# Kernel tuning notes

Measured on AMD Instinct MI355X. Metric: run time of the kernel, lower is better.

The kernel has to match this reference:

```python
import jax, jax.numpy as jnp
import numpy as np

N_NODES = 100000
N_EDGES = 1600000
NODE_IN = 64
EDGE_DIM = 32
NODE_OUT = 64


def setup_inputs() -> dict:
    key = jax.random.key(0)
    ks = jax.random.split(key, 8)
    return {
        "nfeats": jax.random.normal(ks[0], (N_NODES, NODE_IN), dtype=jnp.float32),
        "efeats": jax.random.normal(ks[1], (N_EDGES, EDGE_DIM), dtype=jnp.float32),
        "src": jax.random.randint(ks[2], (N_EDGES,), 0, N_NODES, dtype=jnp.int32),
        "dst": jax.random.randint(ks[3], (N_EDGES,), 0, N_NODES, dtype=jnp.int32),
        "W_msg_w": jax.random.normal(ks[4], (NODE_IN + EDGE_DIM, NODE_OUT), dtype=jnp.float32) * 0.1,
        "W_msg_b": jax.random.normal(ks[5], (NODE_OUT,), dtype=jnp.float32) * 0.1,
        "W_apply_w": jax.random.normal(ks[6], (NODE_IN + NODE_OUT, NODE_OUT), dtype=jnp.float32) * 0.1,
        "W_apply_b": jax.random.normal(ks[7], (NODE_OUT,), dtype=jnp.float32) * 0.1,
    }


def reference(nfeats, efeats, src, dst, W_msg_w, W_msg_b, W_apply_w, W_apply_b):
    n_nodes = nfeats.shape[0]
    # message: gather source node features, concat edge features, linear
    m = jnp.concatenate([nfeats[src], efeats], axis=-1) @ W_msg_w + W_msg_b  # [E, node_out]
    # per-destination mean (DGL fn.mean); zero for isolated nodes
    s = jax.ops.segment_sum(m, dst, num_segments=n_nodes)                     # [N, node_out]
    cnt = jax.ops.segment_sum(jnp.ones((m.shape[0],), m.dtype), dst, num_segments=n_nodes)
    h_neigh = s / jnp.maximum(cnt, 1.0)[:, None]
    # apply: concat self features with aggregated messages, linear, activation
    h = jnp.concatenate([nfeats, h_neigh], axis=-1) @ W_apply_w + W_apply_b   # [N, node_out]
    return jax.nn.relu(h)
```

## Files before the change

### kernel.cpp

```cpp
#include <hip/hip_runtime.h>
#include <hip/hip_bf16.h>

#define NN 100000
#define NE 1600000
#define NBIN 782
#define CAP  2560
#define EPB  8192
#define NBLKE 196

#define OFF_BINSZ   100004
#define OFF_BINBASE 100788
#define OFF_MASK    101572
#define OFF_EINFO   300520
#define OFF_G       3500520
#define OFF_HM      OFF_G
#define OFF_OM      (OFF_G + 153272)
#define OFF_WCOMB   13100520
#define OFF_BMW     13110760

__global__ __launch_bounds__(256) void k_cvt(const float4* __restrict__ nf4,
                                             uint4* __restrict__ nfb) {
  int t = blockIdx.x * 256 + threadIdx.x;
  float4 a = nf4[t * 2], b = nf4[t * 2 + 1];
  uint4 o;
  o.x = ((uint)__bfloat16_as_ushort(__float2bfloat16(a.x))) |
        ((uint)__bfloat16_as_ushort(__float2bfloat16(a.y)) << 16);
  o.y = ((uint)__bfloat16_as_ushort(__float2bfloat16(a.z))) |
        ((uint)__bfloat16_as_ushort(__float2bfloat16(a.w)) << 16);
  o.z = ((uint)__bfloat16_as_ushort(__float2bfloat16(b.x))) |
        ((uint)__bfloat16_as_ushort(__float2bfloat16(b.y)) << 16);
  o.w = ((uint)__bfloat16_as_ushort(__float2bfloat16(b.z))) |
        ((uint)__bfloat16_as_ushort(__float2bfloat16(b.w)) << 16);
  nfb[t] = o;
}

__global__ __launch_bounds__(256) void k_bhist(const int4* __restrict__ dst4,
                                               int* __restrict__ hm) {
  __shared__ int h[NBIN];
  int b = blockIdx.x, t = threadIdx.x;
  for (int i = t; i < NBIN; i += 256) h[i] = 0;
  __syncthreads();
  int e0 = b * EPB;
#pragma unroll
  for (int i = 0; i < EPB / 1024; ++i) {
    int f = i * 256 + t;
    int e = e0 + f * 4;
    if (e < NE) {
      int4 d = dst4[(e0 >> 2) + f];
      atomicAdd(&h[d.x >> 7], 1);
      atomicAdd(&h[d.y >> 7], 1);
      atomicAdd(&h[d.z >> 7], 1);
      atomicAdd(&h[d.w >> 7], 1);
    }
  }
  __syncthreads();
  for (int i = t; i < NBIN; i += 256) hm[b * NBIN + i] = h[i];
}

__global__ __launch_bounds__(256) void k_bscan(const int* __restrict__ hm,
                                               int* __restrict__ om,
                                               int* __restrict__ binsz) {
  int w = (blockIdx.x * 256 + threadIdx.x) >> 6;
  int lane = threadIdx.x & 63;
  if (w >= NBIN) return;
  int carry = 0;
  for (int base = 0; base < NBLKE; base += 64) {
    int b = base + lane;
    int v = (b < NBLKE) ? hm[b * NBIN + w] : 0;
    int inc = v;
#pragma unroll
    for (int off = 1; off < 64; off <<= 1) {
      int x = __shfl_up(inc, off);
      if (lane >= off) inc += x;
    }
    if (b < NBLKE) om[b * NBIN + w] = carry + inc - v;
    carry += __shfl(inc, 63);
  }
  if (lane == 0) binsz[w] = carry;
}

__global__ __launch_bounds__(1024) void k_binscan(const int* __restrict__ binsz,
                                                  int* __restrict__ binbase) {
  __shared__ int s[1024];
  int t = threadIdx.x;
  int v = (t < NBIN) ? binsz[t] : 0;
  s[t] = v; __syncthreads();
#pragma unroll
  for (int off = 1; off < 1024; off <<= 1) {
    int x = (t >= off) ? s[t - off] : 0;
    __syncthreads();
    s[t] += x;
    __syncthreads();
  }
  if (t <= NBIN) binbase[t] = s[t] - v;
}

__global__ __launch_bounds__(256) void k_bplace(
    const int4* __restrict__ src4, const int4* __restrict__ dst4,
    const int* __restrict__ om, const int* __restrict__ binbase,
    int2* __restrict__ einfo) {
  __shared__ int2 buf[EPB];
  __shared__ int hstart[1024];
  __shared__ int hcur[1024];
  __shared__ int obase[NBIN];
  __shared__ int tscan[256];
  int b = blockIdx.x, t = threadIdx.x;
  int e0 = b * EPB;
  for (int i = t; i < 1024; i += 256) hcur[i] = 0;
  for (int i = t; i < NBIN; i += 256) obase[i] = binbase[i] + om[b * NBIN + i];
  __syncthreads();
#pragma unroll
  for (int i = 0; i < EPB / 1024; ++i) {
    int f = i * 256 + t;
    int e = e0 + f * 4;
    if (e < NE) {
      int4 d = dst4[(e0 >> 2) + f];
      atomicAdd(&hcur[d.x >> 7], 1);
      atomicAdd(&hcur[d.y >> 7], 1);
      atomicAdd(&hcur[d.z >> 7], 1);
      atomicAdd(&hcur[d.w >> 7], 1);
    }
  }
  __syncthreads();
  int base4 = t * 4;
  int v0 = hcur[base4], v1 = hcur[base4 + 1], v2 = hcur[base4 + 2], v3 = hcur[base4 + 3];
  int s = v0 + v1 + v2 + v3;
  tscan[t] = s;
  __syncthreads();
#pragma unroll
  for (int off = 1; off < 256; off <<= 1) {
    int x = (t >= off) ? tscan[t - off] : 0;
    __syncthreads();
    tscan[t] += x;
    __syncthreads();
  }
  int texcl = tscan[t] - s;
  hstart[base4]     = texcl;
  hstart[base4 + 1] = texcl + v0;
  hstart[base4 + 2] = texcl + v0 + v1;
  hstart[base4 + 3] = texcl + v0 + v1 + v2;
  __syncthreads();
  for (int i = t; i < 1024; i += 256) hcur[i] = hstart[i];
  __syncthreads();
#pragma unroll
  for (int i = 0; i < EPB / 1024; ++i) {
    int f = i * 256 + t;
    int e = e0 + f * 4;
    if (e < NE) {
      int4 d = dst4[(e0 >> 2) + f];
      int4 sv = src4[(e0 >> 2) + f];
      int p0 = atomicAdd(&hcur[d.x >> 7], 1);
      int p1 = atomicAdd(&hcur[d.y >> 7], 1);
      int p2 = atomicAdd(&hcur[d.z >> 7], 1);
      int p3 = atomicAdd(&hcur[d.w >> 7], 1);
      buf[p0] = make_int2(sv.x | ((d.x & 127) << 20), (e)     | ((d.x >> 7) << 21));
      buf[p1] = make_int2(sv.y | ((d.y & 127) << 20), (e + 1) | ((d.y >> 7) << 21));
      buf[p2] = make_int2(sv.z | ((d.z & 127) << 20), (e + 2) | ((d.z >> 7) << 21));
      buf[p3] = make_int2(sv.w | ((d.w & 127) << 20), (e + 3) | ((d.w >> 7) << 21));
    }
  }
  __syncthreads();
  int nE = NE - e0; if (nE > EPB) nE = EPB;
  for (int i = t; i < nE; i += 256) {
    int2 r = buf[i];
    int bin = (unsigned)r.y >> 21;
    int pos = obase[bin] + (i - hstart[bin]);
    einfo[pos] = make_int2(r.x, r.y & 0x1FFFFF);
  }
}

__global__ __launch_bounds__(512, 8) void k_sortgather(
    const uint* __restrict__ nfb, const float* __restrict__ ef,
    const int2* __restrict__ einfo, const int* __restrict__ binbase,
    float* __restrict__ g, float* __restrict__ mask) {
  __shared__ int2 buf[CAP];
  __shared__ int hist[128];
  __shared__ int excl[128];
  __shared__ int sstart[129];
  int b = blockIdx.x, t = threadIdx.x;
  int base = binbase[b];
  int nE = binbase[b + 1] - base;
  int nS = nE < CAP ? nE : CAP;
  if (t < 128) hist[t] = 0;
  __syncthreads();
  int2 myreg[5];
#pragma unroll
  for (int i = 0; i < 5; ++i) {
    int idx = i * 512 + t;
    if (idx < nS) {
      myreg[i] = einfo[base + idx];
      atomicAdd(&hist[(myreg[i].x >> 20) & 127], 1);
    } else {
      myreg[i] = make_int2(-1, 0);
    }
  }
  __syncthreads();
  int myc = 0;
  if (t < 128) { myc = hist[t]; excl[t] = myc; }
  __syncthreads();
#pragma unroll
  for (int off = 1; off < 128; off <<= 1) {
    int x = 0;
    if (t < 128 && t >= off) x = excl[t - off];
    __syncthreads();
    if (t < 128) excl[t] += x;
    __syncthreads();
  }
  if (t < 128) {
    int node = b * 128 + t;
    if (node < NN) mask[node] = myc ? 1.f : 0.f;
    sstart[t] = excl[t] - myc;
    hist[t] = excl[t] - myc;
    if (t == 127) sstart[128] = excl[127];
  }
  __syncthreads();
#pragma unroll
  for (int i = 0; i < 5; ++i) {
    if (myreg[i].x >= 0) {
      int dl = (myreg[i].x >> 20) & 127;
      int p = atomicAdd(&hist[dl], 1);
      buf[p] = make_int2(myreg[i].x & 0xFFFFF, myreg[i].y);
    }
  }
  __syncthreads();
  int wv = t >> 6, lane = t & 63;
  bool hi = lane >= 32;
  int l32 = lane & 31;
  for (int k = 0; k < 16; ++k) {
    int dl = wv * 16 + k;
    int node = b * 128 + dl;
    if (node >= NN) break;
    int beg = sstart[dl], end = sstart[dl + 1];
    int deg = end - beg;
    float a0x = 0.f, a0y = 0.f, a1 = 0.f;
    int j = beg;
    for (; j + 16 <= end; j += 16) {
      int2 q0 = buf[j + 0];
      int2 q1 = buf[j + 1];
      int2 q2 = buf[j + 2];
      int2 q3 = buf[j + 3];
      int2 q4 = buf[j + 4];
      int2 q5 = buf[j + 5];
      int2 q6 = buf[j + 6];
      int2 q7 = buf[j + 7];
      int2 q8 = buf[j + 8];
      int2 q9 = buf[j + 9];
      int2 qa = buf[j + 10];
      int2 qb = buf[j + 11];
      int2 qc = buf[j + 12];
      int2 qd = buf[j + 13];
      int2 qe = buf[j + 14];
      int2 qf = buf[j + 15];
      int n0 = hi ? q1.x : q0.x;
      int n1 = hi ? q3.x : q2.x;
      int n2 = hi ? q5.x : q4.x;
      int n3 = hi ? q7.x : q6.x;
      int n4 = hi ? q9.x : q8.x;
      int n5 = hi ? qb.x : qa.x;
      int n6 = hi ? qd.x : qc.x;
      int n7 = hi ? qf.x : qe.x;
      int e0 = hi ? q1.y : q0.y;
      int e1 = hi ? q3.y : q2.y;
      int e2 = hi ? q5.y : q4.y;
      int e3 = hi ? q7.y : q6.y;
      int e4 = hi ? q9.y : q8.y;
      int e5 = hi ? qb.y : qa.y;
      int e6 = hi ? qd.y : qc.y;
      int e7 = hi ? qf.y : qe.y;
      uint u0 = nfb[n0 * 32 + l32];
      uint u1 = nfb[n1 * 32 + l32];
      uint u2 = nfb[n2 * 32 + l32];
      uint u3 = nfb[n3 * 32 + l32];
      uint u4 = nfb[n4 * 32 + l32];
      uint u5 = nfb[n5 * 32 + l32];
      uint u6 = nfb[n6 * 32 + l32];
      uint u7 = nfb[n7 * 32 + l32];
      float w0 = ef[e0 * 32 + l32];
      float w1 = ef[e1 * 32 + l32];
      float w2 = ef[e2 * 32 + l32];
      float w3 = ef[e3 * 32 + l32];
      float w4 = ef[e4 * 32 + l32];
      float w5 = ef[e5 * 32 + l32];
      float w6 = ef[e6 * 32 + l32];
      float w7 = ef[e7 * 32 + l32];
      a0x += __uint_as_float(u0 << 16) + __uint_as_float(u1 << 16)
           + __uint_as_float(u2 << 16) + __uint_as_float(u3 << 16)
           + __uint_as_float(u4 << 16) + __uint_as_float(u5 << 16)
           + __uint_as_float(u6 << 16) + __uint_as_float(u7 << 16);
      a0y += __uint_as_float(u0 & 0xFFFF0000u) + __uint_as_float(u1 & 0xFFFF0000u)
           + __uint_as_float(u2 & 0xFFFF0000u) + __uint_as_float(u3 & 0xFFFF0000u)
           + __uint_as_float(u4 & 0xFFFF0000u) + __uint_as_float(u5 & 0xFFFF0000u)
           + __uint_as_float(u6 & 0xFFFF0000u) + __uint_as_float(u7 & 0xFFFF0000u);
      a1 += ((w0 + w1) + (w2 + w3)) + ((w4 + w5) + (w6 + w7));
    }
    for (; j + 8 <= end; j += 8) {
      int2 q0 = buf[j + 0];
      int2 q1 = buf[j + 1];
      int2 q2 = buf[j + 2];
      int2 q3 = buf[j + 3];
      int2 q4 = buf[j + 4];
      int2 q5 = buf[j + 5];
      int2 q6 = buf[j + 6];
      int2 q7 = buf[j + 7];
      int n0 = hi ? q1.x : q0.x;
      int n1 = hi ? q3.x : q2.x;
      int n2 = hi ? q5.x : q4.x;
      int n3 = hi ? q7.x : q6.x;
      int e0 = hi ? q1.y : q0.y;
      int e1 = hi ? q3.y : q2.y;
      int e2 = hi ? q5.y : q4.y;
      int e3 = hi ? q7.y : q6.y;
      uint u0 = nfb[n0 * 32 + l32];
      uint u1 = nfb[n1 * 32 + l32];
      uint u2 = nfb[n2 * 32 + l32];
      uint u3 = nfb[n3 * 32 + l32];
      float w0 = ef[e0 * 32 + l32];
      float w1 = ef[e1 * 32 + l32];
      float w2 = ef[e2 * 32 + l32];
      float w3 = ef[e3 * 32 + l32];
      a0x += __uint_as_float(u0 << 16) + __uint_as_float(u1 << 16)
           + __uint_as_float(u2 << 16) + __uint_as_float(u3 << 16);
      a0y += __uint_as_float(u0 & 0xFFFF0000u) + __uint_as_float(u1 & 0xFFFF0000u)
           + __uint_as_float(u2 & 0xFFFF0000u) + __uint_as_float(u3 & 0xFFFF0000u);
      a1 += (w0 + w1) + (w2 + w3);
    }
    for (; j + 4 <= end; j += 4) {
      int2 q0 = buf[j + 0];
      int2 q1 = buf[j + 1];
      int2 q2 = buf[j + 2];
      int2 q3 = buf[j + 3];
      int n0 = hi ? q1.x : q0.x;
      int n1 = hi ? q3.x : q2.x;
      int e0 = hi ? q1.y : q0.y;
      int e1 = hi ? q3.y : q2.y;
      uint u0 = nfb[n0 * 32 + l32];
      uint u1 = nfb[n1 * 32 + l32];
      float w0 = ef[e0 * 32 + l32];
      float w1 = ef[e1 * 32 + l32];
      a0x += __uint_as_float(u0 << 16) + __uint_as_float(u1 << 16);
      a0y += __uint_as_float(u0 & 0xFFFF0000u) + __uint_as_float(u1 & 0xFFFF0000u);
      a1 += w0 + w1;
    }
    for (; j + 2 <= end; j += 2) {
      int2 q0 = buf[j];
      int2 q1 = buf[j + 1];
      int n0 = hi ? q1.x : q0.x;
      int e0 = hi ? q1.y : q0.y;
      uint u0 = nfb[n0 * 32 + l32];
      float w0 = ef[e0 * 32 + l32];
      a0x += __uint_as_float(u0 << 16);
      a0y += __uint_as_float(u0 & 0xFFFF0000u);
      a1 += w0;
    }
    if (j < end) {
      int2 q0 = buf[j];
      if (!hi) {
        uint u0 = nfb[q0.x * 32 + l32];
        a0x += __uint_as_float(u0 << 16);
        a0y += __uint_as_float(u0 & 0xFFFF0000u);
        a1 += ef[q0.y * 32 + l32];
      }
    }
    a0x += __shfl_xor(a0x, 32);
    a0y += __shfl_xor(a0y, 32);
    a1 += __shfl_down(a1, 32);
    float inv = deg > 0 ? 1.f / (float)deg : 0.f;
    if (!hi) {
      *(float2*)&g[node * 96 + l32 * 2] = make_float2(a0x * inv, a0y * inv);
      g[node * 96 + 64 + l32] = a1 * inv;
    }
  }
}

__global__ __launch_bounds__(256) void k_pre1(
    const float* __restrict__ Wm, const float* __restrict__ bm,
    const float* __restrict__ Wa, float* __restrict__ Wcomb,
    float* __restrict__ bmW) {
  int b = blockIdx.x, t = threadIdx.x;
  if (b < 24) {
    int o = b * 256 + t;
    int k = o >> 6, j = o & 63;
    float acc = 0.f;
    for (int kk = 0; kk < 64; ++kk)
      acc += Wm[k * 64 + kk] * Wa[(64 + kk) * 64 + j];
    Wcomb[(64 + k) * 64 + j] = acc;
  } else {
    for (int i = t; i < 64 * 64; i += 256) Wcomb[i] = Wa[i];
    if (t < 64) {
      float acc = 0.f;
      for (int kk = 0; kk < 64; ++kk) acc += bm[kk] * Wa[(64 + kk) * 64 + t];
      bmW[t] = acc;
    }
  }
}

__global__ __launch_bounds__(256) void k_main(
    const float4* __restrict__ nf4, const float4* __restrict__ g4,
    const float* __restrict__ mask,
    const float4* __restrict__ Wcomb4, const float* __restrict__ bmW,
    const float* __restrict__ ba, float* __restrict__ out) {
  __shared__ float sA[128 * 33];
  __shared__ float sB[32 * 64];
  int tid = threadIdx.x;
  int ty = tid >> 3, tx = tid & 7;
  int nbase = blockIdx.x * 128;
  float acc[4][8];
#pragma unroll
  for (int r = 0; r < 4; ++r)
#pragma unroll
    for (int e = 0; e < 8; ++e) acc[r][e] = 0.f;

  for (int c = 0; c < 5; ++c) {
#pragma unroll
    for (int i = 0; i < 4; ++i) {
      int f = i * 256 + tid;
      int nl = f >> 3, q = f & 7;
      int node = nbase + nl; if (node > NN - 1) node = NN - 1;
      float4 v;
      if (c < 2) {
        v = nf4[node * 16 + c * 8 + q];
      } else {
        v = g4[node * 24 + (c - 2) * 8 + q];
      }
      float* p = &sA[nl * 33 + q * 4];
      p[0] = v.x; p[1] = v.y; p[2] = v.z; p[3] = v.w;
    }
#pragma unroll
    for (int i = 0; i < 2; ++i) {
      int f = i * 256 + tid;
      int kk = f >> 4, j4 = f & 15;
      float4 w = Wcomb4[(c * 32 + kk) * 16 + j4];
      *(float4*)&sB[kk * 64 + j4 * 4] = w;
    }
    __syncthreads();
#pragma unroll 8
    for (int kk = 0; kk < 32; ++kk) {
      float4 b0 = *(const float4*)&sB[kk * 64 + tx * 8];
      float4 b1 = *(const float4*)&sB[kk * 64 + tx * 8 + 4];
#pragma unroll
      for (int r = 0; r < 4; ++r) {
        float a = sA[(ty * 4 + r) * 33 + kk];
        acc[r][0] += a * b0.x; acc[r][1] += a * b0.y;
        acc[r][2] += a * b0.z; acc[r][3] += a * b0.w;
        acc[r][4] += a * b1.x; acc[r][5] += a * b1.y;
        acc[r][6] += a * b1.z; acc[r][7] += a * b1.w;
      }
    }
    __syncthreads();
  }
  float4 ba0 = ((const float4*)ba)[tx * 2];
  float4 ba1 = ((const float4*)ba)[tx * 2 + 1];
  float4 bw0 = ((const float4*)bmW)[tx * 2];
  float4 bw1 = ((const float4*)bmW)[tx * 2 + 1];
#pragma unroll
  for (int r = 0; r < 4; ++r) {
    int node = nbase + ty * 4 + r;
    if (node < NN) {
      float mk = mask[node];
      float4 o0, o1;
      o0.x = acc[r][0] + ba0.x + mk * bw0.x;
      o0.y = acc[r][1] + ba0.y + mk * bw0.y;
      o0.z = acc[r][2] + ba0.z + mk * bw0.z;
      o0.w = acc[r][3] + ba0.w + mk * bw0.w;
      o1.x = acc[r][4] + ba1.x + mk * bw1.x;
      o1.y = acc[r][5] + ba1.y + mk * bw1.y;
      o1.z = acc[r][6] + ba1.z + mk * bw1.z;
      o1.w = acc[r][7] + ba1.w + mk * bw1.w;
      o0.x = fmaxf(o0.x, 0.f); o0.y = fmaxf(o0.y, 0.f);
      o0.z = fmaxf(o0.z, 0.f); o0.w = fmaxf(o0.w, 0.f);
      o1.x = fmaxf(o1.x, 0.f); o1.y = fmaxf(o1.y, 0.f);
      o1.z = fmaxf(o1.z, 0.f); o1.w = fmaxf(o1.w, 0.f);
      *(float4*)&out[node * 64 + tx * 8] = o0;
      *(float4*)&out[node * 64 + tx * 8 + 4] = o1;
    }
  }
}

extern "C" void kernel_launch(void* const* d_in, const int* in_sizes, int n_in,
                              void* d_out, int out_size, void* d_ws, size_t ws_size,
                              hipStream_t stream) {
  const float* nf = (const float*)d_in[0];
  const float* ef = (const float*)d_in[1];
  const int*   src = (const int*)d_in[2];
  const int*   dst = (const int*)d_in[3];
  const float* Wm = (const float*)d_in[4];
  const float* bm = (const float*)d_in[5];
  const float* Wa = (const float*)d_in[6];
  const float* ba = (const float*)d_in[7];
  int*   wsi = (int*)d_ws;
  float* wsf = (float*)d_ws;
  int*   binsz   = wsi + OFF_BINSZ;
  int*   binbase = wsi + OFF_BINBASE;
  int2*  einfo   = (int2*)(wsi + OFF_EINFO);
  int*   hm      = wsi + OFF_HM;
  int*   om      = wsi + OFF_OM;
  float* mask    = wsf + OFF_MASK;
  float* g       = wsf + OFF_G;
  float* Wcomb   = wsf + OFF_WCOMB;
  float* bmW     = wsf + OFF_BMW;
  float* out = (float*)d_out;
  uint*  nfb = (uint*)d_out;

  k_cvt<<<NN * 64 / 8 / 256, 256, 0, stream>>>((const float4*)nf, (uint4*)nfb);
  k_pre1<<<25, 256, 0, stream>>>(Wm, bm, Wa, Wcomb, bmW);
  k_bhist<<<NBLKE, 256, 0, stream>>>((const int4*)dst, hm);
  k_bscan<<<(NBIN * 64 + 255) / 256, 256, 0, stream>>>(hm, om, binsz);
  k_binscan<<<1, 1024, 0, stream>>>(binsz, binbase);
  k_bplace<<<NBLKE, 256, 0, stream>>>((const int4*)src, (const int4*)dst, om,
                                      binbase, einfo);
  k_sortgather<<<NBIN, 512, 0, stream>>>(nfb, ef, einfo, binbase, g, mask);
  k_main<<<(NN + 127) / 128, 256, 0, stream>>>(
      (const float4*)nf, (const float4*)g, mask,
      (const float4*)Wcomb, bmW, ba, out);
}
```

Baseline: 164.1 us.

## Merge front-end kernels into one launch and store aggregated features as bf16

Merges the bf16 conversion, weight pre-combination and destination-bin histogram kernels into one launch, with each block dispatched by its block-index range. This removes two kernel launches and the serialization between them. Separately, the per-node mean aggregates written by the gather kernel become packed bf16 instead of fp32, which halves the intermediate written there and read back by the final GEMM kernel. The narrower storage adds rounding error to the aggregated features, and the final kernel must unpack them when staging into shared memory.

```diff
diff --git a/kernel.cpp b/kernel.cpp
--- a/kernel.cpp
+++ b/kernel.cpp
@@ -7,6 +7,8 @@
 #define CAP  2560
 #define EPB  8192
 #define NBLKE 196
+#define NCVT 3125
+#define NPRE 25
 
 #define OFF_BINSZ   100004
 #define OFF_BINBASE 100788
@@ -18,43 +20,65 @@
 #define OFF_WCOMB   13100520
 #define OFF_BMW     13110760
 
-__global__ __launch_bounds__(256) void k_cvt(const float4* __restrict__ nf4,
-                                             uint4* __restrict__ nfb) {
-  int t = blockIdx.x * 256 + threadIdx.x;
-  float4 a = nf4[t * 2], b = nf4[t * 2 + 1];
-  uint4 o;
-  o.x = ((uint)__bfloat16_as_ushort(__float2bfloat16(a.x))) |
-        ((uint)__bfloat16_as_ushort(__float2bfloat16(a.y)) << 16);
-  o.y = ((uint)__bfloat16_as_ushort(__float2bfloat16(a.z))) |
-        ((uint)__bfloat16_as_ushort(__float2bfloat16(a.w)) << 16);
-  o.z = ((uint)__bfloat16_as_ushort(__float2bfloat16(b.x))) |
-        ((uint)__bfloat16_as_ushort(__float2bfloat16(b.y)) << 16);
-  o.w = ((uint)__bfloat16_as_ushort(__float2bfloat16(b.z))) |
-        ((uint)__bfloat16_as_ushort(__float2bfloat16(b.w)) << 16);
-  nfb[t] = o;
-}
-
-__global__ __launch_bounds__(256) void k_bhist(const int4* __restrict__ dst4,
-                                               int* __restrict__ hm) {
+__device__ __forceinline__ uint packbf(float x, float y) {
+  return ((uint)__bfloat16_as_ushort(__float2bfloat16(x))) |
+         ((uint)__bfloat16_as_ushort(__float2bfloat16(y)) << 16);
+}
+
+__global__ __launch_bounds__(256) void k_front(
+    const float4* __restrict__ nf4, uint4* __restrict__ nfb,
+    const float* __restrict__ Wm, const float* __restrict__ bm,
+    const float* __restrict__ Wa, float* __restrict__ Wcomb,
+    float* __restrict__ bmW,
+    const int4* __restrict__ dst4, int* __restrict__ hm) {
   __shared__ int h[NBIN];
   int b = blockIdx.x, t = threadIdx.x;
-  for (int i = t; i < NBIN; i += 256) h[i] = 0;
-  __syncthreads();
-  int e0 = b * EPB;
-#pragma unroll
-  for (int i = 0; i < EPB / 1024; ++i) {
-    int f = i * 256 + t;
-    int e = e0 + f * 4;
-    if (e < NE) {
-      int4 d = dst4[(e0 >> 2) + f];
-      atomicAdd(&h[d.x >> 7], 1);
-      atomicAdd(&h[d.y >> 7], 1);
-      atomicAdd(&h[d.z >> 7], 1);
-      atomicAdd(&h[d.w >> 7], 1);
-    }
-  }
-  __syncthreads();
-  for (int i = t; i < NBIN; i += 256) hm[b * NBIN + i] = h[i];
+  if (b < NCVT) {
+    int i = b * 256 + t;
+    float4 a = nf4[i * 2], c = nf4[i * 2 + 1];
+    uint4 o;
+    o.x = packbf(a.x, a.y);
+    o.y = packbf(a.z, a.w);
+    o.z = packbf(c.x, c.y);
+    o.w = packbf(c.z, c.w);
+    nfb[i] = o;
+  } else if (b < NCVT + NPRE) {
+    int pb = b - NCVT;
+    if (pb < 24) {
+      int o = pb * 256 + t;
+      int k = o >> 6, j = o & 63;
+      float acc = 0.f;
+      for (int kk = 0; kk < 64; ++kk)
+        acc += Wm[k * 64 + kk] * Wa[(64 + kk) * 64 + j];
+      Wcomb[(64 + k) * 64 + j] = acc;
+    } else {
+      for (int i = t; i < 64 * 64; i += 256) Wcomb[i] = Wa[i];
+      if (t < 64) {
+        float acc = 0.f;
+        for (int kk = 0; kk < 64; ++kk) acc += bm[kk] * Wa[(64 + kk) * 64 + t];
+        bmW[t] = acc;
+      }
+    }
+  } else {
+    int eb = b - NCVT - NPRE;
+    for (int i = t; i < NBIN; i += 256) h[i] = 0;
+    __syncthreads();
+    int e0 = eb * EPB;
+#pragma unroll
+    for (int i = 0; i < EPB / 1024; ++i) {
+      int f = i * 256 + t;
+      int e = e0 + f * 4;
+      if (e < NE) {
+        int4 d = dst4[(e0 >> 2) + f];
+        atomicAdd(&h[d.x >> 7], 1);
+        atomicAdd(&h[d.y >> 7], 1);
+        atomicAdd(&h[d.z >> 7], 1);
+        atomicAdd(&h[d.w >> 7], 1);
+      }
+    }
+    __syncthreads();
+    for (int i = t; i < NBIN; i += 256) hm[eb * NBIN + i] = h[i];
+  }
 }
 
 __global__ __launch_bounds__(256) void k_bscan(const int* __restrict__ hm,
@@ -172,7 +196,7 @@
 __global__ __launch_bounds__(512, 8) void k_sortgather(
     const uint* __restrict__ nfb, const float* __restrict__ ef,
     const int2* __restrict__ einfo, const int* __restrict__ binbase,
-    float* __restrict__ g, float* __restrict__ mask) {
+    uint* __restrict__ gb, float* __restrict__ mask) {
   __shared__ int2 buf[CAP];
   __shared__ int hist[128];
   __shared__ int excl[128];
@@ -365,37 +389,15 @@
     a0y += __shfl_xor(a0y, 32);
     a1 += __shfl_down(a1, 32);
     float inv = deg > 0 ? 1.f / (float)deg : 0.f;
-    if (!hi) {
-      *(float2*)&g[node * 96 + l32 * 2] = make_float2(a0x * inv, a0y * inv);
-      g[node * 96 + 64 + l32] = a1 * inv;
-    }
-  }
-}
-
-__global__ __launch_bounds__(256) void k_pre1(
-    const float* __restrict__ Wm, const float* __restrict__ bm,
-    const float* __restrict__ Wa, float* __restrict__ Wcomb,
-    float* __restrict__ bmW) {
-  int b = blockIdx.x, t = threadIdx.x;
-  if (b < 24) {
-    int o = b * 256 + t;
-    int k = o >> 6, j = o & 63;
-    float acc = 0.f;
-    for (int kk = 0; kk < 64; ++kk)
-      acc += Wm[k * 64 + kk] * Wa[(64 + kk) * 64 + j];
-    Wcomb[(64 + k) * 64 + j] = acc;
-  } else {
-    for (int i = t; i < 64 * 64; i += 256) Wcomb[i] = Wa[i];
-    if (t < 64) {
-      float acc = 0.f;
-      for (int kk = 0; kk < 64; ++kk) acc += bm[kk] * Wa[(64 + kk) * 64 + t];
-      bmW[t] = acc;
-    }
+    float s0 = __shfl(a1, l32 * 2);
+    float s1 = __shfl(a1, l32 * 2 + 1);
+    if (!hi) gb[node * 48 + l32] = packbf(a0x * inv, a0y * inv);
+    if (lane < 16) gb[node * 48 + 32 + lane] = packbf(s0 * inv, s1 * inv);
   }
 }
 
 __global__ __launch_bounds__(256) void k_main(
-    const float4* __restrict__ nf4, const float4* __restrict__ g4,
+    const float4* __restrict__ nf4, const uint4* __restrict__ gb4,
     const float* __restrict__ mask,
     const float4* __restrict__ Wcomb4, const float* __restrict__ bmW,
     const float* __restrict__ ba, float* __restrict__ out) {
@@ -411,19 +413,33 @@
     for (int e = 0; e < 8; ++e) acc[r][e] = 0.f;
 
   for (int c = 0; c < 5; ++c) {
-#pragma unroll
-    for (int i = 0; i < 4; ++i) {
-      int f = i * 256 + tid;
-      int nl = f >> 3, q = f & 7;
-      int node = nbase + nl; if (node > NN - 1) node = NN - 1;
-      float4 v;
-      if (c < 2) {
-        v = nf4[node * 16 + c * 8 + q];
-      } else {
-        v = g4[node * 24 + (c - 2) * 8 + q];
+    if (c < 2) {
+#pragma unroll
+      for (int i = 0; i < 4; ++i) {
+        int f = i * 256 + tid;
+        int nl = f >> 3, q = f & 7;
+        int node = nbase + nl; if (node > NN - 1) node = NN - 1;
+        float4 v = nf4[node * 16 + c * 8 + q];
+        float* p = &sA[nl * 33 + q * 4];
+        p[0] = v.x; p[1] = v.y; p[2] = v.z; p[3] = v.w;
       }
-      float* p = &sA[nl * 33 + q * 4];
-      p[0] = v.x; p[1] = v.y; p[2] = v.z; p[3] = v.w;
+    } else {
+#pragma unroll
+      for (int i = 0; i < 2; ++i) {
+        int f = i * 256 + tid;
+        int nl = f >> 2, qq = f & 3;
+        int node = nbase + nl; if (node > NN - 1) node = NN - 1;
+        uint4 u = gb4[node * 12 + (c - 2) * 4 + qq];
+        float* p = &sA[nl * 33 + qq * 8];
+        p[0] = __uint_as_float(u.x << 16);
+        p[1] = __uint_as_float(u.x & 0xFFFF0000u);
+        p[2] = __uint_as_float(u.y << 16);
+        p[3] = __uint_as_float(u.y & 0xFFFF0000u);
+        p[4] = __uint_as_float(u.z << 16);
+        p[5] = __uint_as_float(u.z & 0xFFFF0000u);
+        p[6] = __uint_as_float(u.w << 16);
+        p[7] = __uint_as_float(u.w & 0xFFFF0000u);
+      }
     }
 #pragma unroll
     for (int i = 0; i < 2; ++i) {
@@ -495,21 +511,21 @@
   int*   hm      = wsi + OFF_HM;
   int*   om      = wsi + OFF_OM;
   float* mask    = wsf + OFF_MASK;
-  float* g       = wsf + OFF_G;
+  uint*  gb      = (uint*)(wsf + OFF_G);
   float* Wcomb   = wsf + OFF_WCOMB;
   float* bmW     = wsf + OFF_BMW;
   float* out = (float*)d_out;
   uint*  nfb = (uint*)d_out;
 
-  k_cvt<<<NN * 64 / 8 / 256, 256, 0, stream>>>((const float4*)nf, (uint4*)nfb);
-  k_pre1<<<25, 256, 0, stream>>>(Wm, bm, Wa, Wcomb, bmW);
-  k_bhist<<<NBLKE, 256, 0, stream>>>((const int4*)dst, hm);
+  k_front<<<NCVT + NPRE + NBLKE, 256, 0, stream>>>(
+      (const float4*)nf, (uint4*)nfb, Wm, bm, Wa, Wcomb, bmW,
+      (const int4*)dst, hm);
   k_bscan<<<(NBIN * 64 + 255) / 256, 256, 0, stream>>>(hm, om, binsz);
   k_binscan<<<1, 1024, 0, stream>>>(binsz, binbase);
   k_bplace<<<NBLKE, 256, 0, stream>>>((const int4*)src, (const int4*)dst, om,
                                       binbase, einfo);
-  k_sortgather<<<NBIN, 512, 0, stream>>>(nfb, ef, einfo, binbase, g, mask);
+  k_sortgather<<<NBIN, 512, 0, stream>>>(nfb, ef, einfo, binbase, gb, mask);
   k_main<<<(NN + 127) / 128, 256, 0, stream>>>(
-      (const float4*)nf, (const float4*)g, mask,
+      (const float4*)nf, (const uint4*)gb, mask,
       (const float4*)Wcomb, bmW, ba, out);
 }
```

After: 151.9 us. 1.08x faster.
